# Kernel optimization log

Measured on AMD Instinct MI355X. Metric: run time of the kernel, lower is better.

The kernel has to match this reference:

```python
import jax, jax.numpy as jnp
import numpy as np

N_WIRES = 10
DEPTH = 2
BATCH = 16384
DIM = 2 ** N_WIRES
N_ENC = min(N_WIRES, 4)


def _cnot_perm(n, c, t):
    # wire 0 is the most-significant bit (torchquantum convention)
    idx = np.arange(2 ** n)
    ctrl = (idx >> (n - 1 - c)) & 1
    return idx ^ (ctrl << (n - 1 - t))


def _ring_perm(n):
    # composition of CNOT(0,1)...CNOT(n-2,n-1), CNOT(n-1,0) as one basis permutation
    perm = np.arange(2 ** n)
    for w in range(n - 1):
        perm = perm[_cnot_perm(n, w, w + 1)]
    perm = perm[_cnot_perm(n, n - 1, 0)]
    return perm


RING_PERM = jnp.asarray(_ring_perm(N_WIRES))
_idx = np.arange(DIM)
# Z_SIGNS[i, w] = +1 if bit of wire w in basis state i is 0, else -1
Z_SIGNS = jnp.asarray(np.stack(
    [1.0 - 2.0 * ((_idx >> (N_WIRES - 1 - w)) & 1) for w in range(N_WIRES)],
    axis=1).astype(np.float32))  # (DIM, N_WIRES)


def _apply_rx(st, cos_h, sin_h, w):
    # RX(theta) = [[cos(t/2), -i sin(t/2)], [-i sin(t/2), cos(t/2)]] on wire w
    # st: (B, DIM) complex64; cos_h/sin_h: scalar (shared param) or (B,) (encoder)
    b = st.shape[0]
    st = st.reshape(b, 2 ** w, 2, -1)
    a0 = st[:, :, 0, :]
    a1 = st[:, :, 1, :]
    c = jnp.reshape(cos_h, (-1, 1, 1))
    s = jnp.reshape(sin_h, (-1, 1, 1))
    n0 = c * a0 - 1j * s * a1
    n1 = -1j * s * a0 + c * a1
    return jnp.stack([n0, n1], axis=2).reshape(b, -1)


def setup_inputs() -> dict:
    key = jax.random.key(0)
    k1, k2 = jax.random.split(key)
    x = jax.random.normal(k1, (BATCH, N_ENC), dtype=jnp.float32)
    theta = 0.1 * jax.random.normal(k2, (N_WIRES,), dtype=jnp.float32)
    return {"x": x, "theta": theta}


def reference(x, theta):
    b = x.shape[0]
    # |0...0> initial state
    st = jnp.zeros((b, DIM), dtype=jnp.complex64).at[:, 0].set(1.0)
    # encoder: RX(x[:, i]) on wire i
    half = x * 0.5
    for i in range(N_ENC):
        st = _apply_rx(st, jnp.cos(half[:, i]), jnp.sin(half[:, i]), i)
    ct = jnp.cos(theta * 0.5)
    sn = jnp.sin(theta * 0.5)
    for _ in range(DEPTH):
        for w in range(N_WIRES):
            st = _apply_rx(st, ct[w], sn[w], w)
        st = st[:, RING_PERM]  # fused CNOT ring
    probs = jnp.real(st * jnp.conj(st))  # (B, DIM)
    return probs @ Z_SIGNS  # (B, N_WIRES) PauliZ expectations
```

## Files before the change

### kernel.cpp

```cpp
#include <hip/hip_runtime.h>
#include <math.h>

#define BATCH 16384
#define NW 10
#define NENC 4
#define DEPTH 2


__global__ __launch_bounds__(256) void k1_basis(const float* __restrict__ theta,
                                                float2* __restrict__ u)
{
    const int lane = threadIdx.x & 63;
    const int a = (blockIdx.x * blockDim.x + threadIdx.x) >> 6;

    float re[16], im[16];
#pragma unroll
    for (int r = 0; r < 16; ++r) { re[r] = 0.0f; im[r] = 0.0f; }
    if (lane == 0) re[a] = 1.0f;

    float ct[NW], st_[NW];
#pragma unroll
    for (int w = 0; w < NW; ++w) {
        const float h = 0.5f * theta[w];
        ct[w] = __cosf(h); st_[w] = __sinf(h);
    }

#pragma unroll 1
    for (int d = 0; d < DEPTH; ++d) {
#pragma unroll
        for (int w = 0; w < 4; ++w) {
            const float c = ct[w], s = st_[w];
            const int m = 8 >> w;
#pragma unroll
            for (int r = 0; r < 16; ++r) {
                if (!(r & m)) {
                    const int r1 = r | m;
                    const float a0r = re[r],  a0i = im[r];
                    const float a1r = re[r1], a1i = im[r1];
                    re[r]  = c * a0r + s * a1i;
                    im[r]  = c * a0i - s * a1r;
                    re[r1] = c * a1r + s * a0i;
                    im[r1] = c * a1i - s * a0r;
                }
            }
        }
#pragma unroll
        for (int w = 4; w < 10; ++w) {
            const float c = ct[w], s = st_[w];
            const int lm = 32 >> (w - 4);
#pragma unroll
            for (int r = 0; r < 16; ++r) {
                const float pr = __shfl_xor(re[r], lm, 64);
                const float pi = __shfl_xor(im[r], lm, 64);
                re[r] = c * re[r] + s * pi;
                im[r] = c * im[r] - s * pr;
            }
        }
#pragma unroll
        for (int w = 0; w < 3; ++w) {
            const int cm = 8 >> w, tm = 8 >> (w + 1);
#pragma unroll
            for (int r = 0; r < 16; ++r) {
                if ((r & cm) && !(r & tm)) {
                    const int r2 = r | tm;
                    float t;
                    t = re[r]; re[r] = re[r2]; re[r2] = t;
                    t = im[r]; im[r] = im[r2]; im[r2] = t;
                }
            }
        }
#pragma unroll
        for (int r = 0; r < 16; ++r) {
            if (r & 1) {
                re[r] = __shfl_xor(re[r], 32, 64);
                im[r] = __shfl_xor(im[r], 32, 64);
            }
        }
#pragma unroll
        for (int w = 4; w < 9; ++w) {
            const int cm = 32 >> (w - 4), tm = 32 >> (w - 3);
            const bool ctl = (lane & cm) != 0;
#pragma unroll
            for (int r = 0; r < 16; ++r) {
                const float pr = __shfl_xor(re[r], tm, 64);
                const float pi = __shfl_xor(im[r], tm, 64);
                re[r] = ctl ? pr : re[r];
                im[r] = ctl ? pi : im[r];
            }
        }
        {
            const bool ctl = (lane & 1) != 0;
#pragma unroll
            for (int r = 0; r < 8; ++r) {
                const float t0r = re[r], t1r = re[r + 8];
                const float t0i = im[r], t1i = im[r + 8];
                re[r]     = ctl ? t1r : t0r;
                re[r + 8] = ctl ? t0r : t1r;
                im[r]     = ctl ? t1i : t0i;
                im[r + 8] = ctl ? t0i : t1i;
            }
        }
    }

#pragma unroll
    for (int r = 0; r < 16; ++r)
        u[a * 1024 + (r << 6) + lane] = make_float2(re[r], im[r]);
}

__global__ __launch_bounds__(256) void k2_gram(const float2* __restrict__ u,
                                               float* __restrict__ C)
{
    const int lane = threadIdx.x & 63;
    const int q = (blockIdx.x * blockDim.x + threadIdx.x) >> 6;
    const int a = q >> 4, b = q & 15;

    float Sr[NW], Si[NW];
#pragma unroll
    for (int w = 0; w < NW; ++w) { Sr[w] = 0.0f; Si[w] = 0.0f; }

#pragma unroll
    for (int t = 0; t < 16; ++t) {
        const int i = t * 64 + lane;
        const float2 ua = u[a * 1024 + i];
        const float2 ub = u[b * 1024 + i];
        const float vr = ua.x * ub.x + ua.y * ub.y;
        const float vi = ua.x * ub.y - ua.y * ub.x;
#pragma unroll
        for (int w = 0; w < NW; ++w) {
            const int mask = 1 << (9 - w);
            const float sv = (i & mask) ? -1.0f : 1.0f;
            Sr[w] = fmaf(sv, vr, Sr[w]);
            Si[w] = fmaf(sv, vi, Si[w]);
        }
    }
#pragma unroll
    for (int w = 0; w < NW; ++w) {
        float r = Sr[w], ii = Si[w];
#pragma unroll
        for (int ofs = 32; ofs >= 1; ofs >>= 1) {
            r  += __shfl_xor(r,  ofs, 64);
            ii += __shfl_xor(ii, ofs, 64);
        }
        Sr[w] = r; Si[w] = ii;
    }

    if (lane == 0) {
        const int p = (__popc(a) - __popc(b)) & 3;
#pragma unroll
        for (int w = 0; w < NW; ++w) {
            const float sr = Sr[w], si = Si[w];
            const float c = (p == 0) ? sr : (p == 1) ? -si : (p == 2) ? -sr : si;
            C[q * 12 + w] = c;
        }
    }
}

__global__ __launch_bounds__(256) void k3_eval(const float* __restrict__ x,
                                               const float* __restrict__ C,
                                               float* __restrict__ out)
{
    __shared__ float lC[256 * 12];
    for (int i = threadIdx.x; i < 256 * 12; i += 256) lC[i] = C[i];
    __syncthreads();

    const int bidx = blockIdx.x * 256 + threadIdx.x;
    const float4 xv = ((const float4*)x)[bidx];

    const float c0 = __cosf(0.5f * xv.x), s0 = __sinf(0.5f * xv.x);
    const float c1 = __cosf(0.5f * xv.y), s1 = __sinf(0.5f * xv.y);
    const float c2 = __cosf(0.5f * xv.z), s2 = __sinf(0.5f * xv.z);
    const float c3 = __cosf(0.5f * xv.w), s3 = __sinf(0.5f * xv.w);

    const float t01[4] = { c0 * c1, c0 * s1, s0 * c1, s0 * s1 };
    const float t23[4] = { c2 * c3, c2 * s3, s2 * c3, s2 * s3 };
    float m[16];
#pragma unroll
    for (int r = 0; r < 16; ++r) m[r] = t01[r >> 2] * t23[r & 3];

    float z[NW];
#pragma unroll
    for (int w = 0; w < NW; ++w) z[w] = 0.0f;

#pragma unroll
    for (int a = 0; a < 16; ++a) {
#pragma unroll
        for (int b = a; b < 16; ++b) {
            const float scale = (a == b) ? 1.0f : 2.0f;
            const float p = scale * m[a] * m[b];
            const float* base = &lC[(a * 16 + b) * 12];
            const float4 q0 = *(const float4*)(base + 0);
            const float4 q1 = *(const float4*)(base + 4);
            const float4 q2 = *(const float4*)(base + 8);
            z[0] = fmaf(p, q0.x, z[0]);
            z[1] = fmaf(p, q0.y, z[1]);
            z[2] = fmaf(p, q0.z, z[2]);
            z[3] = fmaf(p, q0.w, z[3]);
            z[4] = fmaf(p, q1.x, z[4]);
            z[5] = fmaf(p, q1.y, z[5]);
            z[6] = fmaf(p, q1.z, z[6]);
            z[7] = fmaf(p, q1.w, z[7]);
            z[8] = fmaf(p, q2.x, z[8]);
            z[9] = fmaf(p, q2.y, z[9]);
        }
    }

#pragma unroll
    for (int w = 0; w < NW; ++w) out[bidx * NW + w] = z[w];
}

extern "C" void kernel_launch(void* const* d_in, const int* in_sizes, int n_in,
                              void* d_out, int out_size, void* d_ws, size_t ws_size,
                              hipStream_t stream) {
    const float* x     = (const float*)d_in[0];
    const float* theta = (const float*)d_in[1];
    float* out = (float*)d_out;

    float2* u = (float2*)d_ws;
    float*  C = (float*)((char*)d_ws + 16 * 1024 * sizeof(float2));

    hipLaunchKernelGGL(k1_basis, dim3(4),  dim3(256), 0, stream, theta, u);
    hipLaunchKernelGGL(k2_gram,  dim3(64), dim3(256), 0, stream, u, C);
    hipLaunchKernelGGL(k3_eval,  dim3(BATCH / 256), dim3(256), 0, stream, x, C, out);
}
```

Baseline: 79.44 us.

## Reparameterize per-sample evaluation in Fourier basis with precomputed 81-term kernel

Adds a small transform kernel that rewrites the 16x16 Gram coefficients into an 81-term basis over products of {1, cos x, sin x} per encoder wire. The per-sample kernel then computes four full-angle sincos values and does 81 multiply-adds per output instead of 136 pairwise products. It also uses smaller blocks and float2 output stores. The cost is an extra single-block kernel launch on the critical path.

```diff
diff --git a/kernel.cpp b/kernel.cpp
--- a/kernel.cpp
+++ b/kernel.cpp
@@ -155,57 +155,100 @@
     }
 }
 
-__global__ __launch_bounds__(256) void k3_eval(const float* __restrict__ x,
-                                               const float* __restrict__ C,
+__global__ __launch_bounds__(832) void k2b_xform(const float* __restrict__ C,
+                                                 float* __restrict__ K)
+{
+    const int tid = threadIdx.x;
+    if (tid >= 810) return;
+    const int t = tid / 10, w = tid - 10 * t;
+    int d0 = t / 27, r0 = t - d0 * 27;
+    int d1 = r0 / 9, r1 = r0 - d1 * 9;
+    int d2 = r1 / 3, d3 = r1 - d2 * 3;
+    const int d[4] = { d0, d1, d2, d3 };
+
+    float s = 0.0f;
+#pragma unroll
+    for (int e = 0; e < 16; ++e) {
+        int a = 0, b = 0; float sg = 1.0f;
+#pragma unroll
+        for (int q = 0; q < 4; ++q) {
+            const int eq = (e >> (3 - q)) & 1;
+            int aq, bq;
+            if (d[q] == 2) { aq = eq; bq = 1 - eq; }
+            else {
+                aq = eq; bq = eq;
+                if (d[q] == 1 && eq) sg = -sg;
+            }
+            a |= aq << (3 - q);
+            b |= bq << (3 - q);
+        }
+        s += sg * C[(a * 16 + b) * 12 + w];
+    }
+    K[t * 12 + w] = s * 0.0625f;
+}
+
+__global__ __launch_bounds__(128) void k3_eval(const float* __restrict__ x,
+                                               const float* __restrict__ K,
                                                float* __restrict__ out)
 {
-    __shared__ float lC[256 * 12];
-    for (int i = threadIdx.x; i < 256 * 12; i += 256) lC[i] = C[i];
+    __shared__ float lK[81 * 12];
+    for (int i = threadIdx.x; i < 81 * 12; i += 128) lK[i] = K[i];
     __syncthreads();
 
-    const int bidx = blockIdx.x * 256 + threadIdx.x;
+    const int bidx = blockIdx.x * 128 + threadIdx.x;
     const float4 xv = ((const float4*)x)[bidx];
 
-    const float c0 = __cosf(0.5f * xv.x), s0 = __sinf(0.5f * xv.x);
-    const float c1 = __cosf(0.5f * xv.y), s1 = __sinf(0.5f * xv.y);
-    const float c2 = __cosf(0.5f * xv.z), s2 = __sinf(0.5f * xv.z);
-    const float c3 = __cosf(0.5f * xv.w), s3 = __sinf(0.5f * xv.w);
-
-    const float t01[4] = { c0 * c1, c0 * s1, s0 * c1, s0 * s1 };
-    const float t23[4] = { c2 * c3, c2 * s3, s2 * c3, s2 * s3 };
-    float m[16];
-#pragma unroll
-    for (int r = 0; r < 16; ++r) m[r] = t01[r >> 2] * t23[r & 3];
+    float s0, c0, s1, c1, s2, c2, s3, c3;
+    __sincosf(xv.x, &s0, &c0);
+    __sincosf(xv.y, &s1, &c1);
+    __sincosf(xv.z, &s2, &c2);
+    __sincosf(xv.w, &s3, &c3);
+
+    const float b0[3] = { 1.0f, c0, s0 };
+    const float b1[3] = { 1.0f, c1, s1 };
+    const float b2[3] = { 1.0f, c2, s2 };
+    const float b3[3] = { 1.0f, c3, s3 };
+    float B01[9], B23[9];
+#pragma unroll
+    for (int i = 0; i < 3; ++i)
+#pragma unroll
+        for (int j = 0; j < 3; ++j) {
+            B01[i * 3 + j] = b0[i] * b1[j];
+            B23[i * 3 + j] = b2[i] * b3[j];
+        }
 
     float z[NW];
 #pragma unroll
     for (int w = 0; w < NW; ++w) z[w] = 0.0f;
 
 #pragma unroll
-    for (int a = 0; a < 16; ++a) {
-#pragma unroll
-        for (int b = a; b < 16; ++b) {
-            const float scale = (a == b) ? 1.0f : 2.0f;
-            const float p = scale * m[a] * m[b];
-            const float* base = &lC[(a * 16 + b) * 12];
+    for (int t01 = 0; t01 < 9; ++t01) {
+#pragma unroll
+        for (int t23 = 0; t23 < 9; ++t23) {
+            const float P = B01[t01] * B23[t23];
+            const float* base = &lK[(t01 * 9 + t23) * 12];
             const float4 q0 = *(const float4*)(base + 0);
             const float4 q1 = *(const float4*)(base + 4);
             const float4 q2 = *(const float4*)(base + 8);
-            z[0] = fmaf(p, q0.x, z[0]);
-            z[1] = fmaf(p, q0.y, z[1]);
-            z[2] = fmaf(p, q0.z, z[2]);
-            z[3] = fmaf(p, q0.w, z[3]);
-            z[4] = fmaf(p, q1.x, z[4]);
-            z[5] = fmaf(p, q1.y, z[5]);
-            z[6] = fmaf(p, q1.z, z[6]);
-            z[7] = fmaf(p, q1.w, z[7]);
-            z[8] = fmaf(p, q2.x, z[8]);
-            z[9] = fmaf(p, q2.y, z[9]);
-        }
-    }
-
-#pragma unroll
-    for (int w = 0; w < NW; ++w) out[bidx * NW + w] = z[w];
+            z[0] = fmaf(P, q0.x, z[0]);
+            z[1] = fmaf(P, q0.y, z[1]);
+            z[2] = fmaf(P, q0.z, z[2]);
+            z[3] = fmaf(P, q0.w, z[3]);
+            z[4] = fmaf(P, q1.x, z[4]);
+            z[5] = fmaf(P, q1.y, z[5]);
+            z[6] = fmaf(P, q1.z, z[6]);
+            z[7] = fmaf(P, q1.w, z[7]);
+            z[8] = fmaf(P, q2.x, z[8]);
+            z[9] = fmaf(P, q2.y, z[9]);
+        }
+    }
+
+    float2* po = (float2*)(out + bidx * NW);
+    po[0] = make_float2(z[0], z[1]);
+    po[1] = make_float2(z[2], z[3]);
+    po[2] = make_float2(z[4], z[5]);
+    po[3] = make_float2(z[6], z[7]);
+    po[4] = make_float2(z[8], z[9]);
 }
 
 extern "C" void kernel_launch(void* const* d_in, const int* in_sizes, int n_in,
@@ -217,8 +260,10 @@
 
     float2* u = (float2*)d_ws;
     float*  C = (float*)((char*)d_ws + 16 * 1024 * sizeof(float2));
-
-    hipLaunchKernelGGL(k1_basis, dim3(4),  dim3(256), 0, stream, theta, u);
-    hipLaunchKernelGGL(k2_gram,  dim3(64), dim3(256), 0, stream, u, C);
-    hipLaunchKernelGGL(k3_eval,  dim3(BATCH / 256), dim3(256), 0, stream, x, C, out);
-}
+    float*  K = C + 256 * 12;
+
+    hipLaunchKernelGGL(k1_basis,  dim3(4),   dim3(256), 0, stream, theta, u);
+    hipLaunchKernelGGL(k2_gram,   dim3(64),  dim3(256), 0, stream, u, C);
+    hipLaunchKernelGGL(k2b_xform, dim3(1),   dim3(832), 0, stream, C, K);
+    hipLaunchKernelGGL(k3_eval,   dim3(BATCH / 128), dim3(128), 0, stream, x, K, out);
+}
```

Measured after the change: 80.34 us. About the same (+1.1%).
